# Kernel optimization log

Hardware: AMD Instinct MI355X
Metric: run time of the kernel (lower is better)

The kernel has to match this reference:

```python
import jax, jax.numpy as jnp
import numpy as np

B, L, S, D, H, E, UV = 4, 2048, 2048, 1024, 8, 128, 128
ROT_DIM = H * E  # RotaryEmbedding(dim=qk_size*n_heads) applied on flattened dim


def gelu(x):
    return jax.nn.gelu(x, approximate=False)  # torch nn.GELU default (erf)


def rope(x):
    # x: [B, T, ROT_DIM]; interleaved-pair rotary (lucidrains rotary_embedding_torch default)
    T = x.shape[1]
    inv_freq = 1.0 / (10000.0 ** (jnp.arange(0, ROT_DIM, 2, dtype=jnp.float32) / ROT_DIM))
    freqs = jnp.arange(T, dtype=jnp.float32)[:, None] * inv_freq  # [T, ROT_DIM/2]
    cos = jnp.repeat(jnp.cos(freqs), 2, axis=-1)  # [T, ROT_DIM]
    sin = jnp.repeat(jnp.sin(freqs), 2, axis=-1)
    xp = x.reshape(*x.shape[:-1], ROT_DIM // 2, 2)
    x_rot = jnp.stack([-xp[..., 1], xp[..., 0]], axis=-1).reshape(x.shape)
    return x * cos + x_rot * sin


def setup_inputs() -> dict:
    key = jax.random.key(0)
    ks = jax.random.split(key, 16)
    n = lambda k, sh, s=1.0: jax.random.normal(k, sh, jnp.float32) * s
    w = 0.02
    return {
        "u": n(ks[0], (B, L, D)),
        "queries": n(ks[1], (B, L, D)),
        "keys": n(ks[2], (B, S, D)),
        "values": n(ks[3], (B, S, D)),
        "Wqk": n(ks[4], (D, H * E), w), "bqk": jnp.zeros((H * E,), jnp.float32),
        "Wv": n(ks[5], (D, H * UV), w), "bv": jnp.zeros((H * UV,), jnp.float32),
        "Wu": n(ks[6], (D, H * UV), w), "bu": jnp.zeros((H * UV,), jnp.float32),
        "Wo": n(ks[7], (H * UV, D), w), "bo": jnp.zeros((D,), jnp.float32),
        "q_gamma": jnp.ones((E,), jnp.float32), "q_beta": n(ks[8], (E,), w),
        "k_gamma": jnp.ones((E,), jnp.float32), "k_beta": n(ks[9], (E,), w),
    }


def _forward(u, queries, keys, values, Wqk, bqk, Wv, bv, Wu, bu, Wo, bo,
             q_gamma, q_beta, k_gamma, k_beta):
    # use_aff=True: shared qk projection + per-branch ScaleOffset over qk_size
    qk = gelu(queries @ Wqk + bqk)                      # [B,L,H*E]
    qk4 = qk.reshape(B, L, H, E)
    q = (qk4 * q_gamma + q_beta).reshape(B, L, H * E)
    k = (qk4 * k_gamma + k_beta).reshape(B, L, H * E)
    q = rope(q).reshape(B, L, H, E)
    k = rope(k).reshape(B, S, H, E)
    v = gelu(values @ Wv + bv).reshape(B, S, H, UV)
    # Conv1d(kernel_size=1) == pointwise linear over channels
    u_p = gelu(u @ Wu + bu).reshape(B, L, H, UV)
    scale = 1.0 / jnp.sqrt(jnp.float32(E))
    scores = jnp.einsum("blhe,bshe->bhls", q, k) * scale
    attn = jax.nn.softmax(scores, axis=-1)              # [B,H,L,S]
    ctx = jnp.einsum("bhls,bshd->blhd", attn, v)        # [B,L,H,UV]
    out = (u_p * ctx).reshape(B, L, H * UV)             # gate by u
    o = out @ Wo + bo                                   # [B,L,D]
    return o, attn


def reference(u, queries, keys, values, Wqk, bqk, Wv, bv, Wu, bu, Wo, bo,
              q_gamma, q_beta, k_gamma, k_beta):
    return _forward(u, queries, keys, values, Wqk, bqk, Wv, bv, Wu, bu, Wo, bo,
                    q_gamma, q_beta, k_gamma, k_beta)
```

## Files before the change

kernel.cpp:

```cpp
#include <hip/hip_runtime.h>
#include <hip/hip_bf16.h>
#include <math.h>

#define DEVI static __device__ __forceinline__

typedef __attribute__((ext_vector_type(4))) float f32x4;
typedef __attribute__((ext_vector_type(16))) float f32x16;
typedef __attribute__((ext_vector_type(8))) short bf16x8;
typedef __attribute__((ext_vector_type(4))) short bf16x4;

constexpr int Bc = 4, Lc = 2048, Sc = 2048, Dc = 1024, Hc = 8, Ec = 128, UVc = 128;
constexpr int HEc = Hc * Ec;
constexpr int BLc = Bc * Lc;

#define QSC (1.44269504088896340f / 11.31370849898476039f)

DEVI unsigned f2bf_bits(float f) {
  unsigned u = __builtin_bit_cast(unsigned, f);
  return (u + 0x7FFFu + ((u >> 16) & 1u)) >> 16;
}
DEVI short f2bf(float f) { return (short)f2bf_bits(f); }
DEVI float bf2f(short s) {
  return __builtin_bit_cast(float, (unsigned)((unsigned short)s) << 16);
}
DEVI float gelu_f(float x) { return 0.5f * x * (1.0f + erff(x * 0.7071067811865476f)); }

DEVI void gload16(const void* gsrc, void* ldst) {
  __builtin_amdgcn_global_load_lds(
      (const __attribute__((address_space(1))) unsigned*)gsrc,
      (__attribute__((address_space(3))) unsigned*)(ldst), 16, 0, 0);
}

DEVI f32x4 mfma16(bf16x8 a, bf16x8 b, f32x4 c) {
  return __builtin_amdgcn_mfma_f32_16x16x32_bf16(a, b, c, 0, 0, 0);
}
DEVI f32x16 mfma32(bf16x8 a, bf16x8 b, f32x16 c) {
  return __builtin_amdgcn_mfma_f32_32x32x16_bf16(a, b, c, 0, 0, 0);
}

__global__ void cvt3_kernel(const float* __restrict__ i0, const float* __restrict__ i1,
                            const float* __restrict__ i2, short* __restrict__ o0,
                            short* __restrict__ o1, short* __restrict__ o2) {
  const float* ins[3] = {i0, i1, i2};
  short* outs[3] = {o0, o1, o2};
  const float* in = ins[blockIdx.y];
  short* out = outs[blockIdx.y];
  size_t i = ((size_t)blockIdx.x * 256 + threadIdx.x) * 8;
  float4 f1 = *reinterpret_cast<const float4*>(in + i);
  float4 f2 = *reinterpret_cast<const float4*>(in + i + 4);
  uint4 pk;
  pk.x = f2bf_bits(f1.x) | (f2bf_bits(f1.y) << 16);
  pk.y = f2bf_bits(f1.z) | (f2bf_bits(f1.w) << 16);
  pk.z = f2bf_bits(f2.x) | (f2bf_bits(f2.y) << 16);
  pk.w = f2bf_bits(f2.z) | (f2bf_bits(f2.w) << 16);
  *reinterpret_cast<uint4*>(out + i) = pk;
}

__global__ void wt_trans_kernel(const float* __restrict__ W0, const float* __restrict__ W1,
                                const float* __restrict__ W2, const float* __restrict__ W3,
                                short* __restrict__ T0, short* __restrict__ T1,
                                short* __restrict__ T2, short* __restrict__ T3) {
  __shared__ float t[32][33];
  const float* Ws[4] = {W0, W1, W2, W3};
  short* Ts[4] = {T0, T1, T2, T3};
  const float* W = Ws[blockIdx.z];
  short* WT = Ts[blockIdx.z];
  int tx = threadIdx.x, ty = threadIdx.y;
  int n0 = blockIdx.x * 32, k0 = blockIdx.y * 32;
#pragma unroll
  for (int i = 0; i < 4; i++) {
    int r = ty + i * 8;
    t[r][tx] = W[(size_t)(k0 + r) * 1024 + n0 + tx];
  }
  __syncthreads();
#pragma unroll
  for (int i = 0; i < 4; i++) {
    int r = ty + i * 8;
    WT[(size_t)(n0 + r) * 1024 + k0 + tx] = f2bf(t[tx][r]);
  }
}

__global__ void rope_cs_kernel(float2* __restrict__ cs) {
  int idx = blockIdx.x * 256 + threadIdx.x;
  int t = idx >> 9, i = idx & 511;
  float inv = expf((float)i * (-9.210340371976184f / 512.0f));
  float sv, cv;
  sincosf((float)t * inv, &sv, &cv);
  cs[idx] = make_float2(cv, sv);
}

template <int EPI>
__global__ __launch_bounds__(256, 3) void gemm_kernel(
    const short* __restrict__ A, const short* __restrict__ BT,
    const float* __restrict__ bias, void* __restrict__ Cptr, int M, int N, int K) {
  __shared__ char smem[49152];
  const int tid = threadIdx.x;
  const int wave = tid >> 6, lane = tid & 63;
  const int lquad = lane >> 4, l15 = lane & 15;
  const int m0 = blockIdx.x * 128, n0 = blockIdx.y * 128;
  const int wr = wave >> 1, wc = wave & 1;
  f32x4 acc[4][4] = {};

  const int q0 = tid * 16, q1 = tid * 16 + 4096;
  const int r0 = q0 >> 6, o0 = (q0 & 63) ^ ((r0 & 3) << 4);
  const int r1 = q1 >> 6, o1 = (q1 & 63) ^ ((r1 & 3) << 4);
  const short* a0 = A + (size_t)(m0 + r0) * K + (o0 >> 1);
  const short* a1 = A + (size_t)(m0 + r1) * K + (o1 >> 1);
  const short* b0 = BT + (size_t)(n0 + r0) * K + (o0 >> 1);
  const short* b1 = BT + (size_t)(n0 + r1) * K + (o1 >> 1);

#define G_STAGE(buf, kt)                     \
  {                                          \
    char* As_ = smem + (buf)*8192;           \
    char* Bs_ = smem + 24576 + (buf)*8192;   \
    gload16(a0 + (kt), As_ + q0);            \
    gload16(a1 + (kt), As_ + q1);            \
    gload16(b0 + (kt), Bs_ + q0);            \
    gload16(b1 + (kt), Bs_ + q1);            \
  }

  G_STAGE(0, 0);
  G_STAGE(1, 32);
  asm volatile("s_waitcnt vmcnt(4)" ::: "memory");
  __builtin_amdgcn_s_barrier();

  const int NT = K >> 5;
  int cur = 0;
  for (int t = 0; t < NT; t++) {
    int nb = cur + 2;
    if (nb >= 3) nb -= 3;
    G_STAGE(nb, (t + 2 < NT) ? (t + 2) * 32 : 0);
    __builtin_amdgcn_sched_barrier(0);
    const char* As_ = smem + cur * 8192;
    const char* Bs_ = smem + 24576 + cur * 8192;
    const int ko = lquad * 16;
    bf16x8 a[4], b[4];
#pragma unroll
    for (int f = 0; f < 4; f++) {
      int ra = wr * 64 + f * 16 + l15;
      a[f] = *reinterpret_cast<const bf16x8*>(As_ + ra * 64 + (ko ^ ((ra & 3) << 4)));
      int rb = wc * 64 + f * 16 + l15;
      b[f] = *reinterpret_cast<const bf16x8*>(Bs_ + rb * 64 + (ko ^ ((rb & 3) << 4)));
    }
#pragma unroll
    for (int mf = 0; mf < 4; mf++)
#pragma unroll
      for (int nf = 0; nf < 4; nf++)
        acc[mf][nf] = mfma16(a[mf], b[nf], acc[mf][nf]);
    asm volatile("s_waitcnt vmcnt(4) lgkmcnt(0)" ::: "memory");
    __builtin_amdgcn_sched_barrier(0);
    __builtin_amdgcn_s_barrier();
    cur = (cur == 2) ? 0 : cur + 1;
  }
#undef G_STAGE

#pragma unroll
  for (int mf = 0; mf < 4; mf++) {
#pragma unroll
    for (int nf = 0; nf < 4; nf++) {
      const int mrow = m0 + wr * 64 + mf * 16 + 4 * lquad;
      const int ncol = n0 + wc * 64 + nf * 16 + l15;
      const float bval = bias[ncol];
      if constexpr (EPI == 3) {
        int hh = ncol >> 7, dd = ncol & 127;
        int bb = mrow >> 11, ss = mrow & 2047;
        bf16x4 gv;
#pragma unroll
        for (int r = 0; r < 4; r++) gv[r] = f2bf(gelu_f(acc[mf][nf][r] + bval));
        *reinterpret_cast<bf16x4*>((short*)Cptr + (((size_t)bb * 8 + hh) * 128 + dd) * 2048 + ss) = gv;
      } else if constexpr (EPI == 1) {
#pragma unroll
        for (int r = 0; r < 4; r++)
          ((short*)Cptr)[(size_t)(mrow + r) * N + ncol] = f2bf(gelu_f(acc[mf][nf][r] + bval));
      } else {
#pragma unroll
        for (int r = 0; r < 4; r++)
          ((float*)Cptr)[(size_t)(mrow + r) * N + ncol] = acc[mf][nf][r] + bval;
      }
    }
  }
}

__global__ void rope_apply_kernel(const short* __restrict__ qkg,
                                  const float2* __restrict__ cstab,
                                  const float* __restrict__ qg, const float* __restrict__ qb,
                                  const float* __restrict__ kg, const float* __restrict__ kb,
                                  short* __restrict__ qo, short* __restrict__ ko) {
  int tid = blockIdx.x * 256 + threadIdx.x;
  size_t base = (size_t)tid * 8;
  int bl = (int)(base >> 10);
  int rem = (int)(base & 1023);
  int e0 = rem & 127;
  int t = bl & 2047;
  int pf = rem >> 1;
  uint4 raw = *reinterpret_cast<const uint4*>(qkg + base);
  short sh[8];
  *reinterpret_cast<uint4*>(sh) = raw;
  const float* csf = (const float*)cstab + (size_t)t * 1024 + 2 * pf;
  float4 p01 = *reinterpret_cast<const float4*>(csf);
  float4 p23 = *reinterpret_cast<const float4*>(csf + 4);
  float C[4] = {p01.x, p01.z, p23.x, p23.z};
  float Sn[4] = {p01.y, p01.w, p23.y, p23.w};
  float4 qga = *reinterpret_cast<const float4*>(qg + e0);
  float4 qgb = *reinterpret_cast<const float4*>(qg + e0 + 4);
  float4 qba = *reinterpret_cast<const float4*>(qb + e0);
  float4 qbb = *reinterpret_cast<const float4*>(qb + e0 + 4);
  float4 kga = *reinterpret_cast<const float4*>(kg + e0);
  float4 kgb = *reinterpret_cast<const float4*>(kg + e0 + 4);
  float4 kba = *reinterpret_cast<const float4*>(kb + e0);
  float4 kbb = *reinterpret_cast<const float4*>(kb + e0 + 4);
  float QG[8] = {qga.x, qga.y, qga.z, qga.w, qgb.x, qgb.y, qgb.z, qgb.w};
  float QB[8] = {qba.x, qba.y, qba.z, qba.w, qbb.x, qbb.y, qbb.z, qbb.w};
  float KG[8] = {kga.x, kga.y, kga.z, kga.w, kgb.x, kgb.y, kgb.z, kgb.w};
  float KB[8] = {kba.x, kba.y, kba.z, kba.w, kbb.x, kbb.y, kbb.z, kbb.w};
  short qsh[8], ksh[8];
#pragma unroll
  for (int j = 0; j < 4; j++) {
    float x0 = bf2f(sh[2 * j]), x1 = bf2f(sh[2 * j + 1]);
    float q0 = x0 * QG[2 * j] + QB[2 * j];
    float q1 = x1 * QG[2 * j + 1] + QB[2 * j + 1];
    qsh[2 * j] = f2bf((q0 * C[j] - q1 * Sn[j]) * QSC);
    qsh[2 * j + 1] = f2bf((q1 * C[j] + q0 * Sn[j]) * QSC);
    float k0v = x0 * KG[2 * j] + KB[2 * j];
    float k1v = x1 * KG[2 * j + 1] + KB[2 * j + 1];
    ksh[2 * j] = f2bf(k0v * C[j] - k1v * Sn[j]);
    ksh[2 * j + 1] = f2bf(k1v * C[j] + k0v * Sn[j]);
  }
  *reinterpret_cast<uint4*>(qo + base) = *reinterpret_cast<uint4*>(qsh);
  *reinterpret_cast<uint4*>(ko + base) = *reinterpret_cast<uint4*>(ksh);
}

__global__ __launch_bounds__(256, 3) void passa_kernel(
    const short* __restrict__ qs, const short* __restrict__ ks,
    float* __restrict__ rcpbuf) {
  __shared__ char smem[49152];
  const int bid = blockIdx.x;
  const int xcd = bid & 7, jj = bid >> 3;
  const int bh = xcd * 4 + (jj >> 4);
  const int lblk = jj & 15;
  const int b = bh >> 3, h = bh & 7;
  const int l0 = lblk * 128;
  const int tid = threadIdx.x;
  const int wave = tid >> 6, lane = tid & 63;
  const int l31 = lane & 31, lhg = lane >> 5;

  const short* ksrc[4];
  int kq[4];
#pragma unroll
  for (int i = 0; i < 4; i++) {
    int q = i * 4096 + tid * 16;
    kq[i] = q;
    int row = q >> 8, off = (q & 255) ^ ((row & 7) << 4);
    ksrc[i] = ks + (((size_t)b * Sc + row) * Hc + h) * Ec + (off >> 1);
  }

  bf16x8 qf[8];
  {
    const char* qp = (const char*)(qs + (((size_t)b * Lc + l0 + wave * 32 + l31) * Hc + h) * Ec);
#pragma unroll
    for (int kt = 0; kt < 8; kt++)
      qf[kt] = *reinterpret_cast<const bf16x8*>(qp + kt * 32 + 16 * lhg);
  }
  __builtin_amdgcn_sched_barrier(0);

#define STAGE_A(buf, s0)                                  \
  {                                                       \
    char* Kb_ = smem + (buf)*16384;                       \
    gload16(ksrc[0] + (size_t)(s0)*1024, Kb_ + kq[0]);    \
    gload16(ksrc[1] + (size_t)(s0)*1024, Kb_ + kq[1]);    \
    gload16(ksrc[2] + (size_t)(s0)*1024, Kb_ + kq[2]);    \
    gload16(ksrc[3] + (size_t)(s0)*1024, Kb_ + kq[3]);    \
  }

  STAGE_A(0, 0);
  STAGE_A(1, 64);
  asm volatile("s_waitcnt vmcnt(4)" ::: "memory");
  __builtin_amdgcn_s_barrier();
  float ra = 0.f, rb = 0.f, rc = 0.f, rd = 0.f;
  int cur = 0;
  for (int t = 0; t < 32; t++) {
    int nb = cur + 2;
    if (nb >= 3) nb -= 3;
    STAGE_A(nb, (t + 2 < 32) ? (t + 2) * 64 : 0);
    __builtin_amdgcn_sched_barrier(0);
    const char* KB_ = smem + cur * 16384;
    f32x16 d0 = {}, d1 = {};
    __builtin_amdgcn_s_setprio(1);
#pragma unroll
    for (int kt = 0; kt < 8; kt++) {
      int row0 = l31, row1 = 32 + l31;
      bf16x8 k0 = *reinterpret_cast<const bf16x8*>(
          KB_ + row0 * 256 + ((kt * 32 + 16 * lhg) ^ ((row0 & 7) << 4)));
      bf16x8 k1 = *reinterpret_cast<const bf16x8*>(
          KB_ + row1 * 256 + ((kt * 32 + 16 * lhg) ^ ((row1 & 7) << 4)));
      d0 = mfma32(k0, qf[kt], d0);
      d1 = mfma32(k1, qf[kt], d1);
    }
    __builtin_amdgcn_s_setprio(0);
#pragma unroll
    for (int r = 0; r < 16; r += 4) {
      ra += exp2f(d0[r]) + exp2f(d1[r]);
      rb += exp2f(d0[r + 1]) + exp2f(d1[r + 1]);
      rc += exp2f(d0[r + 2]) + exp2f(d1[r + 2]);
      rd += exp2f(d0[r + 3]) + exp2f(d1[r + 3]);
    }
    asm volatile("s_waitcnt vmcnt(4) lgkmcnt(0)" ::: "memory");
    __builtin_amdgcn_sched_barrier(0);
    __builtin_amdgcn_s_barrier();
    cur = (cur == 2) ? 0 : cur + 1;
  }
#undef STAGE_A
  float rs = (ra + rb) + (rc + rd);
  rs += __shfl_xor(rs, 32);
  if (lane < 32)
    rcpbuf[(size_t)bh * Lc + l0 + wave * 32 + l31] = 1.0f / rs;
}

__global__ __launch_bounds__(256, 3) void attn_kernel(
    const short* __restrict__ qs, const short* __restrict__ ks,
    const short* __restrict__ vT, const short* __restrict__ up,
    const float* __restrict__ rcpbuf, float* __restrict__ attn_out,
    short* __restrict__ gate) {
  __shared__ char smem[49152];
  const int bid = blockIdx.x;
  const int xcd = bid & 7, jj = bid >> 3;
  const int bh = xcd * 4 + (jj >> 5);
  const int lblk = jj & 31;
  const int b = bh >> 3, h = bh & 7;
  const int l0 = lblk * 64;
  const int tid = threadIdx.x;
  const int wave = tid >> 6, lane = tid & 63;
  const int lquad = lane >> 4, l15 = lane & 15;

  const short* ksrc[2];
  int kq[2];
#pragma unroll
  for (int i = 0; i < 2; i++) {
    int q = i * 4096 + tid * 16;
    kq[i] = q;
    int row = q >> 8, off = (q & 255) ^ ((row & 7) << 4);
    ksrc[i] = ks + (((size_t)b * Sc + row) * Hc + h) * Ec + (off >> 1);
  }
  const short* vsrc[2];
  int vq[2];
#pragma unroll
  for (int i = 0; i < 2; i++) {
    int q = i * 4096 + tid * 16;
    vq[i] = q;
    int rv = q >> 6;
    int j = (q >> 4) & 3;
    int c = (j - (rv & 3)) & 3;
    vsrc[i] = vT + ((size_t)bh * UVc + rv) * Sc + (c << 3);
  }

  bf16x8 qf[4];
  {
    int lrow = l0 + wave * 16 + l15;
    const short* qp = qs + (((size_t)b * Lc + lrow) * Hc + h) * Ec;
#pragma unroll
    for (int kt = 0; kt < 4; kt++)
      qf[kt] = *reinterpret_cast<const bf16x8*>(qp + kt * 32 + lquad * 8);
  }
  const float rcp = rcpbuf[(size_t)bh * Lc + l0 + wave * 16 + l15];
  __builtin_amdgcn_sched_barrier(0);

#define STAGE_B(buf, s0)                                  \
  {                                                       \
    char* Kb_ = smem + (buf)*8192;                        \
    char* Vb_ = smem + 24576 + (buf)*8192;                \
    gload16(ksrc[0] + (size_t)(s0)*1024, Kb_ + kq[0]);    \
    gload16(ksrc[1] + (size_t)(s0)*1024, Kb_ + kq[1]);    \
    gload16(vsrc[0] + (s0), Vb_ + vq[0]);                 \
    gload16(vsrc[1] + (s0), Vb_ + vq[1]);                 \
  }

  STAGE_B(0, 0);
  STAGE_B(1, 32);
  asm volatile("s_waitcnt vmcnt(4)" ::: "memory");
  __builtin_amdgcn_s_barrier();
  f32x4 ctx[8] = {};
  int cur = 0;
  for (int t = 0; t < 64; t++) {
    const int s0 = t * 32;
    int nb = cur + 2;
    if (nb >= 3) nb -= 3;
    STAGE_B(nb, (t + 2 < 64) ? s0 + 64 : 0);
    __builtin_amdgcn_sched_barrier(0);
    const char* KB_ = smem + cur * 8192;
    const char* VB_ = smem + 24576 + cur * 8192;
    f32x4 d[2] = {};
    __builtin_amdgcn_s_setprio(1);
#pragma unroll
    for (int kt = 0; kt < 4; kt++)
#pragma unroll
      for (int sf = 0; sf < 2; sf++) {
        int row = sf * 16 + l15;
        bf16x8 kf = *reinterpret_cast<const bf16x8*>(
            KB_ + row * 256 + ((kt * 64 + lquad * 16) ^ ((row & 7) << 4)));
        d[sf] = mfma16(kf, qf[kt], d[sf]);
      }
    __builtin_amdgcn_s_setprio(0);
#pragma unroll
    for (int sf = 0; sf < 2; sf++)
#pragma unroll
      for (int r = 0; r < 4; r++)
        d[sf][r] = exp2f(d[sf][r]) * rcp;
    {
      int lrow = l0 + wave * 16 + l15;
      float* arow = attn_out + ((size_t)bh * Lc + lrow) * Sc + s0 + lquad * 4;
      __builtin_nontemporal_store(d[0], reinterpret_cast<f32x4*>(arow));
      __builtin_nontemporal_store(d[1], reinterpret_cast<f32x4*>(arow + 16));
    }
    bf16x8 pb;
#pragma unroll
    for (int r = 0; r < 4; r++) {
      pb[r] = f2bf(d[0][r]);
      pb[4 + r] = f2bf(d[1][r]);
    }
    __builtin_amdgcn_s_setprio(1);
#pragma unroll
    for (int df = 0; df < 8; df++) {
      int dd = df * 16 + l15;
      const char* vrow = VB_ + dd * 64;
      int half = (lquad & 1) * 8;
      int clo = ((lquad >> 1) + (dd & 3)) & 3;
      int chi = ((lquad >> 1) + 2 + (dd & 3)) & 3;
      bf16x4 lo = *reinterpret_cast<const bf16x4*>(vrow + clo * 16 + half);
      bf16x4 hi = *reinterpret_cast<const bf16x4*>(vrow + chi * 16 + half);
      bf16x8 vf = __builtin_shufflevector(lo, hi, 0, 1, 2, 3, 4, 5, 6, 7);
      ctx[df] = mfma16(vf, pb, ctx[df]);
    }
    __builtin_amdgcn_s_setprio(0);
    asm volatile("s_waitcnt vmcnt(6) lgkmcnt(0)" ::: "memory");
    __builtin_amdgcn_sched_barrier(0);
    __builtin_amdgcn_s_barrier();
    cur = (cur == 2) ? 0 : cur + 1;
  }
#undef STAGE_B

  {
    int lrow = l0 + wave * 16 + l15;
    size_t base = ((size_t)b * Lc + lrow) * HEc + h * UVc;
    const short* ub = up + base;
    short* gp = gate + base;
#pragma unroll
    for (int df = 0; df < 8; df++) {
      int doff = df * 16 + lquad * 4;
      bf16x4 uv = *reinterpret_cast<const bf16x4*>(ub + doff);
      bf16x4 gv;
#pragma unroll
      for (int r = 0; r < 4; r++)
        gv[r] = f2bf(bf2f(uv[r]) * ctx[df][r]);
      *reinterpret_cast<bf16x4*>(gp + doff) = gv;
    }
  }
}

extern "C" void kernel_launch(void* const* d_in, const int* in_sizes, int n_in,
                              void* d_out, int out_size, void* d_ws, size_t ws_size,
                              hipStream_t stream) {
  const float* u_in = (const float*)d_in[0];
  const float* qry = (const float*)d_in[1];
  const float* vals = (const float*)d_in[3];
  const float* Wqk = (const float*)d_in[4];
  const float* bqk = (const float*)d_in[5];
  const float* Wv = (const float*)d_in[6];
  const float* bv = (const float*)d_in[7];
  const float* Wu = (const float*)d_in[8];
  const float* bu = (const float*)d_in[9];
  const float* Wo = (const float*)d_in[10];
  const float* bo = (const float*)d_in[11];
  const float* qg = (const float*)d_in[12];
  const float* qb = (const float*)d_in[13];
  const float* kg = (const float*)d_in[14];
  const float* kb = (const float*)d_in[15];

  char* w = (char*)d_ws;
  short* WT0 = (short*)w; w += (size_t)1024 * 1024 * 2;
  short* WT1 = (short*)w; w += (size_t)1024 * 1024 * 2;
  short* WT2 = (short*)w; w += (size_t)1024 * 1024 * 2;
  short* WT3 = (short*)w; w += (size_t)1024 * 1024 * 2;
  float2* cstab = (float2*)w; w += (size_t)2048 * 512 * 8;
  float* rcpb = (float*)w; w += (size_t)32 * 2048 * 4;
  const size_t BUF = (size_t)BLc * HEc * 2;
  short* C1 = (short*)w; w += BUF;
  short* C2 = (short*)w; w += BUF;
  short* C3 = (short*)w; w += BUF;
  short* qkg = (short*)w; w += BUF;
  short* qbf = (short*)w; w += BUF;
  short* vTb = (short*)w; w += BUF;
  short* upb = (short*)w; w += BUF;
  short* kbf = qkg;
  short* gtb = C1;

  float* o_out = (float*)d_out;
  float* attn_out = o_out + (size_t)BLc * Dc;

  dim3 tb(32, 8);
  cvt3_kernel<<<dim3(4096, 3), 256, 0, stream>>>(qry, vals, u_in, C1, C2, C3);
  wt_trans_kernel<<<dim3(32, 32, 4), tb, 0, stream>>>(Wqk, Wv, Wu, Wo, WT0, WT1, WT2, WT3);
  rope_cs_kernel<<<4096, 256, 0, stream>>>(cstab);

  gemm_kernel<1><<<dim3(64, 8), 256, 0, stream>>>(C1, WT0, bqk, qkg, BLc, HEc, Dc);
  rope_apply_kernel<<<4096, 256, 0, stream>>>(qkg, cstab, qg, qb, kg, kb, qbf, kbf);
  passa_kernel<<<512, 256, 0, stream>>>(qbf, kbf, rcpb);
  gemm_kernel<3><<<dim3(64, 8), 256, 0, stream>>>(C2, WT1, bv, vTb, BLc, HEc, Dc);
  gemm_kernel<1><<<dim3(64, 8), 256, 0, stream>>>(C3, WT2, bu, upb, BLc, HEc, Dc);
  attn_kernel<<<1024, 256, 0, stream>>>(qbf, kbf, vTb, upb, rcpb, attn_out, gtb);
  gemm_kernel<0><<<dim3(64, 8), 256, 0, stream>>>(gtb, WT3, bo, o_out, BLc, Dc, HEc);
}
```

Baseline: 390.4 us.

## Double query rows per attention block to reuse K/V tiles across two fragments

Each attention block now covers 128 query rows instead of 64, and each wave handles two 16-row fragments that share every K and V fragment read from LDS. The grid is halved to 512 blocks, so K/V global loads and LDS reads per query row are cut in half. In exchange, accumulator and Q-fragment register use doubles, which may lower occupancy under the 3-blocks launch bound. With fewer blocks there is also less parallelism across the GPU's compute units.

Measured after the change: 391.3 us. No clear change (+0.2%).

```diff
diff --git a/kernel.cpp b/kernel.cpp
--- a/kernel.cpp
+++ b/kernel.cpp
@@ -324,10 +324,10 @@
   __shared__ char smem[49152];
   const int bid = blockIdx.x;
   const int xcd = bid & 7, jj = bid >> 3;
-  const int bh = xcd * 4 + (jj >> 5);
-  const int lblk = jj & 31;
+  const int bh = xcd * 4 + (jj >> 4);
+  const int lblk = jj & 15;
   const int b = bh >> 3, h = bh & 7;
-  const int l0 = lblk * 64;
+  const int l0 = lblk * 128;
   const int tid = threadIdx.x;
   const int wave = tid >> 6, lane = tid & 63;
   const int lquad = lane >> 4, l15 = lane & 15;
@@ -353,15 +353,17 @@
     vsrc[i] = vT + ((size_t)bh * UVc + rv) * Sc + (c << 3);
   }
 
-  bf16x8 qf[4];
-  {
-    int lrow = l0 + wave * 16 + l15;
+  bf16x8 qf[2][4];
+  float rcp[2];
+#pragma unroll
+  for (int cf = 0; cf < 2; cf++) {
+    int lrow = l0 + wave * 32 + cf * 16 + l15;
     const short* qp = qs + (((size_t)b * Lc + lrow) * Hc + h) * Ec;
 #pragma unroll
     for (int kt = 0; kt < 4; kt++)
-      qf[kt] = *reinterpret_cast<const bf16x8*>(qp + kt * 32 + lquad * 8);
-  }
-  const float rcp = rcpbuf[(size_t)bh * Lc + l0 + wave * 16 + l15];
+      qf[cf][kt] = *reinterpret_cast<const bf16x8*>(qp + kt * 32 + lquad * 8);
+    rcp[cf] = rcpbuf[(size_t)bh * Lc + lrow];
+  }
   __builtin_amdgcn_sched_barrier(0);
 
 #define STAGE_B(buf, s0)                                  \
@@ -378,7 +380,7 @@
   STAGE_B(1, 32);
   asm volatile("s_waitcnt vmcnt(4)" ::: "memory");
   __builtin_amdgcn_s_barrier();
-  f32x4 ctx[8] = {};
+  f32x4 ctx[8][2] = {};
   int cur = 0;
   for (int t = 0; t < 64; t++) {
     const int s0 = t * 32;
@@ -388,7 +390,7 @@
     __builtin_amdgcn_sched_barrier(0);
     const char* KB_ = smem + cur * 8192;
     const char* VB_ = smem + 24576 + cur * 8192;
-    f32x4 d[2] = {};
+    f32x4 d[2][2] = {};
     __builtin_amdgcn_s_setprio(1);
 #pragma unroll
     for (int kt = 0; kt < 4; kt++)
@@ -397,26 +399,32 @@
         int row = sf * 16 + l15;
         bf16x8 kf = *reinterpret_cast<const bf16x8*>(
             KB_ + row * 256 + ((kt * 64 + lquad * 16) ^ ((row & 7) << 4)));
-        d[sf] = mfma16(kf, qf[kt], d[sf]);
+        d[sf][0] = mfma16(kf, qf[0][kt], d[sf][0]);
+        d[sf][1] = mfma16(kf, qf[1][kt], d[sf][1]);
       }
     __builtin_amdgcn_s_setprio(0);
 #pragma unroll
     for (int sf = 0; sf < 2; sf++)
 #pragma unroll
-      for (int r = 0; r < 4; r++)
-        d[sf][r] = exp2f(d[sf][r]) * rcp;
-    {
-      int lrow = l0 + wave * 16 + l15;
+      for (int cf = 0; cf < 2; cf++)
+#pragma unroll
+        for (int r = 0; r < 4; r++)
+          d[sf][cf][r] = exp2f(d[sf][cf][r]) * rcp[cf];
+#pragma unroll
+    for (int cf = 0; cf < 2; cf++) {
+      int lrow = l0 + wave * 32 + cf * 16 + l15;
       float* arow = attn_out + ((size_t)bh * Lc + lrow) * Sc + s0 + lquad * 4;
-      __builtin_nontemporal_store(d[0], reinterpret_cast<f32x4*>(arow));
-      __builtin_nontemporal_store(d[1], reinterpret_cast<f32x4*>(arow + 16));
-    }
-    bf16x8 pb;
-#pragma unroll
-    for (int r = 0; r < 4; r++) {
-      pb[r] = f2bf(d[0][r]);
-      pb[4 + r] = f2bf(d[1][r]);
-    }
+      __builtin_nontemporal_store(d[0][cf], reinterpret_cast<f32x4*>(arow));
+      __builtin_nontemporal_store(d[1][cf], reinterpret_cast<f32x4*>(arow + 16));
+    }
+    bf16x8 pb[2];
+#pragma unroll
+    for (int cf = 0; cf < 2; cf++)
+#pragma unroll
+      for (int r = 0; r < 4; r++) {
+        pb[cf][r] = f2bf(d[0][cf][r]);
+        pb[cf][4 + r] = f2bf(d[1][cf][r]);
+      }
     __builtin_amdgcn_s_setprio(1);
 #pragma unroll
     for (int df = 0; df < 8; df++) {
@@ -428,7 +436,8 @@
       bf16x4 lo = *reinterpret_cast<const bf16x4*>(vrow + clo * 16 + half);
       bf16x4 hi = *reinterpret_cast<const bf16x4*>(vrow + chi * 16 + half);
       bf16x8 vf = __builtin_shufflevector(lo, hi, 0, 1, 2, 3, 4, 5, 6, 7);
-      ctx[df] = mfma16(vf, pb, ctx[df]);
+      ctx[df][0] = mfma16(vf, pb[0], ctx[df][0]);
+      ctx[df][1] = mfma16(vf, pb[1], ctx[df][1]);
     }
     __builtin_amdgcn_s_setprio(0);
     asm volatile("s_waitcnt vmcnt(6) lgkmcnt(0)" ::: "memory");
@@ -438,8 +447,9 @@
   }
 #undef STAGE_B
 
-  {
-    int lrow = l0 + wave * 16 + l15;
+#pragma unroll
+  for (int cf = 0; cf < 2; cf++) {
+    int lrow = l0 + wave * 32 + cf * 16 + l15;
     size_t base = ((size_t)b * Lc + lrow) * HEc + h * UVc;
     const short* ub = up + base;
     short* gp = gate + base;
@@ -450,7 +460,7 @@
       bf16x4 gv;
 #pragma unroll
       for (int r = 0; r < 4; r++)
-        gv[r] = f2bf(bf2f(uv[r]) * ctx[df][r]);
+        gv[r] = f2bf(bf2f(uv[r]) * ctx[df][cf][r]);
       *reinterpret_cast<bf16x4*>(gp + doff) = gv;
     }
   }
@@ -506,6 +516,6 @@
   passa_kernel<<<512, 256, 0, stream>>>(qbf, kbf, rcpb);
   gemm_kernel<3><<<dim3(64, 8), 256, 0, stream>>>(C2, WT1, bv, vTb, BLc, HEc, Dc);
   gemm_kernel<1><<<dim3(64, 8), 256, 0, stream>>>(C3, WT2, bu, upb, BLc, HEc, Dc);
-  attn_kernel<<<1024, 256, 0, stream>>>(qbf, kbf, vTb, upb, rcpb, attn_out, gtb);
+  attn_kernel<<<512, 256, 0, stream>>>(qbf, kbf, vTb, upb, rcpb, attn_out, gtb);
   gemm_kernel<0><<<dim3(64, 8), 256, 0, stream>>>(gtb, WT3, bo, o_out, BLc, Dc, HEc);
 }
```
